# Performance work log

Hardware: AMD Instinct MI355X
Metric: run time of the kernel (lower is better)

## Reference

```python
import jax, jax.numpy as jnp
import numpy as np

E = 500_000
NODE_DIM = 128
EDGE_DIM = 128
GLOB_DIM = 64
NUM_GRAPHS = 64
HIDDEN = 4 * EDGE_DIM  # 512
IN_DIM = 2 * NODE_DIM + EDGE_DIM + GLOB_DIM  # 448
EPS = 1e-5


def setup_inputs() -> dict:
    key = jax.random.key(0)
    ks = jax.random.split(key, 12)
    src = jax.random.normal(ks[0], (E, NODE_DIM), dtype=jnp.float32)
    dest = jax.random.normal(ks[1], (E, NODE_DIM), dtype=jnp.float32)
    edge_attr = jax.random.normal(ks[2], (E, EDGE_DIM), dtype=jnp.float32)
    u = jax.random.normal(ks[3], (NUM_GRAPHS, GLOB_DIM), dtype=jnp.float32)
    batch = jnp.sort(jax.random.randint(ks[4], (E,), 0, NUM_GRAPHS, dtype=jnp.int32))
    # MLP params (kaiming-ish scale)
    W1 = jax.random.normal(ks[5], (IN_DIM, HIDDEN), dtype=jnp.float32) / np.sqrt(IN_DIM)
    b1 = jnp.zeros((HIDDEN,), dtype=jnp.float32)
    W2 = jax.random.normal(ks[6], (HIDDEN, EDGE_DIM), dtype=jnp.float32) / np.sqrt(HIDDEN)
    b2 = jnp.zeros((EDGE_DIM,), dtype=jnp.float32)
    # GraphNorm params
    gn_weight = jnp.ones((EDGE_DIM,), dtype=jnp.float32)
    gn_bias = jnp.zeros((EDGE_DIM,), dtype=jnp.float32)
    mean_scale = jnp.ones((EDGE_DIM,), dtype=jnp.float32)
    return {"src": src, "dest": dest, "edge_attr": edge_attr, "u": u, "batch": batch,
            "W1": W1, "b1": b1, "W2": W2, "b2": b2,
            "gn_weight": gn_weight, "gn_bias": gn_bias, "mean_scale": mean_scale}


def _graph_norm(x, batch, weight, bias, mean_scale):
    # per-graph mean
    cnt = jax.ops.segment_sum(jnp.ones((x.shape[0],), x.dtype), batch, num_segments=NUM_GRAPHS)
    cnt = jnp.maximum(cnt, 1.0)[:, None]  # [G,1]
    mean = jax.ops.segment_sum(x, batch, num_segments=NUM_GRAPHS) / cnt  # [G,D]
    out = x - mean[batch] * mean_scale
    var = jax.ops.segment_sum(out * out, batch, num_segments=NUM_GRAPHS) / cnt  # [G,D]
    std = jnp.sqrt(var + EPS)
    return out / std[batch] * weight + bias


def reference(src, dest, edge_attr, u, batch, W1, b1, W2, b2, gn_weight, gn_bias, mean_scale):
    # gather per-graph globals + concat: [E, 2*node+edge+glob]
    h = jnp.concatenate([src, dest, edge_attr, u[batch]], axis=1)
    h = jax.nn.relu(h @ W1 + b1) @ W2 + b2  # [E, edge_dim]
    out = _graph_norm(h + edge_attr, batch, gn_weight, gn_bias, mean_scale)
    return out  # dropout is identity in eval / p=0.0
```

## Files before the change

kernel.cpp:

```cpp
#include <hip/hip_runtime.h>
#include <hip/hip_bf16.h>
#include <stdint.h>

#define E_EDGES   500000
#define MBLK      32
#define NBLK      15625
#define EPSV      1e-5f

typedef unsigned short u16;
typedef __attribute__((ext_vector_type(8))) short short8;
typedef __attribute__((ext_vector_type(4))) float f32x4;
typedef __attribute__((ext_vector_type(2))) uint32_t u32x2;

__device__ __forceinline__ u16 f2bf(float f) {
  __hip_bfloat16 h = __float2bfloat16(f);
  return *(u16*)&h;
}
__device__ __forceinline__ uint32_t pk2bf(float lo, float hi) {
  return (uint32_t)f2bf(lo) | ((uint32_t)f2bf(hi) << 16);
}

__global__ void prep_weights(const float* __restrict__ W1, const float* __restrict__ W2,
                             u16* __restrict__ w1f, u16* __restrict__ w2f) {
  int idx = blockIdx.x * blockDim.x + threadIdx.x;
  if (idx < 32*14*64) {
    int lane = idx & 63; int t = idx >> 6; int k32 = t % 14; int n16 = t / 14;
    int n = n16*16 + (lane & 15); int k0 = k32*32 + (lane >> 4)*8;
    short8 pk;
#pragma unroll
    for (int j = 0; j < 8; ++j) pk[j] = (short)f2bf(W1[(size_t)(k0 + j)*512 + n]);
    *(short8*)&w1f[(size_t)idx * 8] = pk;
  } else if (idx < 32*14*64 + 8*16*64) {
    int i2 = idx - 32*14*64;
    int lane = i2 & 63; int t = i2 >> 6; int k32 = t % 16; int n16 = t / 16;
    int n = n16*16 + (lane & 15); int k0 = k32*32 + (lane >> 4)*8;
    short8 pk;
#pragma unroll
    for (int j = 0; j < 8; ++j) pk[j] = (short)f2bf(W2[(size_t)(k0 + j)*128 + n]);
    *(short8*)&w2f[(size_t)i2 * 8] = pk;
  }
}

#define SWZ16(row, byte) ((byte) ^ (((row) & 7) << 4))

__global__ __launch_bounds__(256, 4)
void fused_kernel(const float* __restrict__ srcp, const float* __restrict__ destp,
                  const float* __restrict__ edgep, const float* __restrict__ up,
                  const int* __restrict__ batch, const float* __restrict__ b1,
                  const float* __restrict__ b2,
                  const u16* __restrict__ w1f, const u16* __restrict__ w2f,
                  float* __restrict__ outp,
                  float* __restrict__ sums0, float* __restrict__ sums2,
                  float* __restrict__ cntsh, int nshard) {
  const int tid  = threadIdx.x;
  const int lane = tid & 63;
  const int w    = tid >> 6;
  const int l15  = lane & 15, l4 = lane >> 4;

  __shared__ __align__(16) u16 lds[32*512];
  char* ldsb = (char*)lds;

  const long grow0 = (long)blockIdx.x * MBLK;

  {
    const int srow = tid >> 3;
    const int c8   = (tid & 7) * 8;
    const long sgrow = grow0 + srow;
    const int  bat = batch[sgrow];
#pragma unroll
    for (int j = 0; j < 7; ++j) {
      const float* sp;
      if (j == 0)      sp = srcp  + sgrow*128 + c8;
      else if (j == 1) sp = srcp  + sgrow*128 + 64 + c8;
      else if (j == 2) sp = destp + sgrow*128 + c8;
      else if (j == 3) sp = destp + sgrow*128 + 64 + c8;
      else if (j == 4) sp = edgep + sgrow*128 + c8;
      else if (j == 5) sp = edgep + sgrow*128 + 64 + c8;
      else             sp = up + (size_t)bat*64 + c8;
      f32x4 t0 = *(const f32x4*)(sp);
      f32x4 t1 = *(const f32x4*)(sp + 4);
      u32x2 lohi0 = (u32x2){pk2bf(t0[0], t0[1]), pk2bf(t0[2], t0[3])};
      u32x2 lohi1 = (u32x2){pk2bf(t1[0], t1[1]), pk2bf(t1[2], t1[3])};
      char* dst = ldsb + srow*896 + SWZ16(srow, (j*64 + c8)*2);
      *(u32x2*)(dst)     = lohi0;
      *(u32x2*)(dst + 8) = lohi1;
    }
  }
  __syncthreads();

  f32x4 acc1[2][8];
#pragma unroll
  for (int nj = 0; nj < 8; ++nj) {
    float bv = b1[(w*8 + nj)*16 + l15];
    acc1[0][nj] = (f32x4){bv, bv, bv, bv};
    acc1[1][nj] = (f32x4){bv, bv, bv, bv};
  }

#pragma unroll
  for (int k32 = 0; k32 < 14; ++k32) {
    short8 a[2], b[8];
#pragma unroll
    for (int mi = 0; mi < 2; ++mi) {
      int row = mi*16 + l15;
      a[mi] = *(const short8*)(ldsb + row*896 + SWZ16(row, k32*64 + l4*16));
    }
#pragma unroll
    for (int nj = 0; nj < 8; ++nj)
      b[nj] = *(const short8*)&w1f[((size_t)((w*8 + nj)*14 + k32)*64 + lane)*8];
    __builtin_amdgcn_s_setprio(1);
#pragma unroll
    for (int mi = 0; mi < 2; ++mi)
#pragma unroll
      for (int nj = 0; nj < 8; ++nj)
        acc1[mi][nj] = __builtin_amdgcn_mfma_f32_16x16x32_bf16(a[mi], b[nj], acc1[mi][nj], 0, 0, 0);
    __builtin_amdgcn_s_setprio(0);
  }
  __syncthreads();

#pragma unroll
  for (int nj = 0; nj < 8; ++nj) {
    int n = (w*8 + nj)*16 + l15;
#pragma unroll
    for (int mi = 0; mi < 2; ++mi)
#pragma unroll
      for (int rr = 0; rr < 4; ++rr) {
        int row = mi*16 + l4*4 + rr;
        *(u16*)(ldsb + row*1024 + SWZ16(row, n*2)) = f2bf(fmaxf(acc1[mi][nj][rr], 0.f));
      }
  }
  __syncthreads();

  const int c4    = tid & 31;
  const int rbase = tid >> 5;
  f32x4 ebuf[4];
#pragma unroll
  for (int p = 0; p < 4; ++p)
    ebuf[p] = *(const f32x4*)(edgep + (grow0 + rbase + p*8)*128 + c4*4);

  f32x4 acc2[2][2];
#pragma unroll
  for (int nj = 0; nj < 2; ++nj) {
    float bv = b2[(w*2 + nj)*16 + l15];
    acc2[0][nj] = (f32x4){bv, bv, bv, bv};
    acc2[1][nj] = (f32x4){bv, bv, bv, bv};
  }

#pragma unroll
  for (int kb = 0; kb < 16; ++kb) {
    short8 hb[2], wfr[2];
#pragma unroll
    for (int mi = 0; mi < 2; ++mi) {
      int row = mi*16 + l15;
      hb[mi] = *(const short8*)(ldsb + row*1024 + SWZ16(row, kb*64 + l4*16));
    }
#pragma unroll
    for (int nj = 0; nj < 2; ++nj)
      wfr[nj] = *(const short8*)&w2f[(((size_t)((w*2 + nj)*16 + kb))*64 + lane)*8];
    __builtin_amdgcn_s_setprio(1);
#pragma unroll
    for (int mi = 0; mi < 2; ++mi)
#pragma unroll
      for (int nj = 0; nj < 2; ++nj)
        acc2[mi][nj] = __builtin_amdgcn_mfma_f32_16x16x32_bf16(hb[mi], wfr[nj], acc2[mi][nj], 0, 0, 0);
    __builtin_amdgcn_s_setprio(0);
  }
  __syncthreads();

#pragma unroll
  for (int mi = 0; mi < 2; ++mi)
#pragma unroll
    for (int nj = 0; nj < 2; ++nj) {
      int col = (w*2 + nj)*16 + l15;
#pragma unroll
      for (int rr = 0; rr < 4; ++rr) {
        int row = mi*16 + l4*4 + rr;
        *(float*)(ldsb + row*512 + SWZ16(row, col*4)) = acc2[mi][nj][rr];
      }
    }
  __syncthreads();

  const int g0 = batch[grow0];
  const int g1 = batch[grow0 + MBLK - 1];
  const int sh = blockIdx.x & (nshard - 1);

  if (g0 == g1) {
    f32x4 s = (f32x4){0,0,0,0}, s2 = (f32x4){0,0,0,0};
#pragma unroll
    for (int p = 0; p < 4; ++p) {
      int row = rbase + p*8;
      f32x4 y = *(const f32x4*)(ldsb + row*512 + SWZ16(row, c4*16));
      y = y + ebuf[p];
      *(f32x4*)(outp + (grow0 + row)*128 + c4*4) = y;
      s = s + y; s2 = s2 + y*y;
    }
    int slot = 16384 + (rbase*32 + c4)*32;
    *(f32x4*)(ldsb + slot)      = s;
    *(f32x4*)(ldsb + slot + 16) = s2;
    __syncthreads();
    int c4r = tid >> 3, stat = (tid >> 2) & 1, cq = tid & 3;
    float v = 0.f;
#pragma unroll
    for (int r = 0; r < 8; ++r)
      v += *(const float*)(ldsb + 16384 + (r*32 + c4r)*32 + stat*16 + cq*4);
    float* dst = stat ? sums2 : sums0;
    atomicAdd(&dst[(size_t)sh*8192 + g0*128 + c4r*4 + cq], v);
    if (tid == 0) atomicAdd(&cntsh[sh*64 + g0], (float)MBLK);
  } else {
    f32x4 s = (f32x4){0,0,0,0}, s2 = (f32x4){0,0,0,0};
    float rc = 0.f; int gcur = -1;
#pragma unroll
    for (int p = 0; p < 4; ++p) {
      int row = rbase + p*8;
      int g = batch[grow0 + row];
      if (g != gcur) {
        if (gcur >= 0) {
#pragma unroll
          for (int c = 0; c < 4; ++c) {
            atomicAdd(&sums0[(size_t)sh*8192 + gcur*128 + c4*4 + c], s[c]);
            atomicAdd(&sums2[(size_t)sh*8192 + gcur*128 + c4*4 + c], s2[c]);
          }
          if (c4 == 0) atomicAdd(&cntsh[sh*64 + gcur], rc);
        }
        gcur = g; s = (f32x4){0,0,0,0}; s2 = (f32x4){0,0,0,0}; rc = 0.f;
      }
      f32x4 y = *(const f32x4*)(ldsb + row*512 + SWZ16(row, c4*16));
      y = y + ebuf[p];
      *(f32x4*)(outp + (grow0 + row)*128 + c4*4) = y;
      s = s + y; s2 = s2 + y*y; rc += 1.f;
    }
#pragma unroll
    for (int c = 0; c < 4; ++c) {
      atomicAdd(&sums0[(size_t)sh*8192 + gcur*128 + c4*4 + c], s[c]);
      atomicAdd(&sums2[(size_t)sh*8192 + gcur*128 + c4*4 + c], s2[c]);
    }
    if (c4 == 0) atomicAdd(&cntsh[sh*64 + gcur], rc);
  }
}

__global__ void finalize_kernel(const float* __restrict__ sums0, const float* __restrict__ sums2,
                                const float* __restrict__ cntsh, int nshard,
                                const float* __restrict__ gnw, const float* __restrict__ gnb,
                                const float* __restrict__ ms,
                                float* __restrict__ scale, float* __restrict__ shift) {
  int idx = blockIdx.x*blockDim.x + threadIdx.x;
  if (idx >= 64*128) return;
  int g = idx >> 7, d = idx & 127;
  float s = 0.f, s2 = 0.f, c = 0.f;
  for (int sh = 0; sh < nshard; ++sh) {
    s  += sums0[(size_t)sh*8192 + idx];
    s2 += sums2[(size_t)sh*8192 + idx];
    c  += cntsh[sh*64 + g];
  }
  c = fmaxf(c, 1.0f);
  float mean = s / c;
  float mm = mean * ms[d];
  float var = fmaxf(s2 / c - 2.f*mm*mean + mm*mm, 0.f);
  float sc = gnw[d] / sqrtf(var + EPSV);
  scale[idx] = sc;
  shift[idx] = gnb[d] - mm*sc;
}

__global__ void norm_kernel(float* __restrict__ y, const int* __restrict__ batch,
                            const float* __restrict__ scale, const float* __restrict__ shift) {
  long i = (long)blockIdx.x*blockDim.x + threadIdx.x;
  const long n4 = (long)E_EDGES * 32;
  long stride = (long)gridDim.x*blockDim.x;
  for (; i < n4; i += stride) {
    long row = i >> 5;
    int dq = (int)(i & 31) << 2;
    int g = batch[row];
    f32x4 v = *(f32x4*)(y + i*4);
    f32x4 sc = *(const f32x4*)(scale + g*128 + dq);
    f32x4 sh = *(const f32x4*)(shift + g*128 + dq);
    v = v*sc + sh;
    *(f32x4*)(y + i*4) = v;
  }
}

extern "C" void kernel_launch(void* const* d_in, const int* in_sizes, int n_in,
                              void* d_out, int out_size, void* d_ws, size_t ws_size,
                              hipStream_t stream) {
  const float* srcp  = (const float*)d_in[0];
  const float* destp = (const float*)d_in[1];
  const float* edgep = (const float*)d_in[2];
  const float* up    = (const float*)d_in[3];
  const int*   batch = (const int*)d_in[4];
  const float* W1    = (const float*)d_in[5];
  const float* b1    = (const float*)d_in[6];
  const float* W2    = (const float*)d_in[7];
  const float* b2    = (const float*)d_in[8];
  const float* gnw   = (const float*)d_in[9];
  const float* gnb   = (const float*)d_in[10];
  const float* ms    = (const float*)d_in[11];
  float* outp = (float*)d_out;

  char* ws = (char*)d_ws;
  u16*   w1f   = (u16*)(ws + 0);
  u16*   w2f   = (u16*)(ws + 458752);
  float* scale = (float*)(ws + 589824);
  float* shift = (float*)(ws + 622592);
  float* cntsh = (float*)(ws + 655360);
  int nshard = 32;
  while (nshard > 1 && 663552 + (size_t)nshard*65536 > ws_size) nshard >>= 1;
  float* sums0 = (float*)(ws + 663552);
  float* sums2 = (float*)(ws + 663552 + (size_t)nshard*32768);

  hipMemsetAsync(ws + 655360, 0, 8192 + (size_t)nshard*65536, stream);
  prep_weights<<<dim3(144), dim3(256), 0, stream>>>(W1, W2, w1f, w2f);

  fused_kernel<<<dim3(NBLK), dim3(256), 0, stream>>>(srcp, destp, edgep, up, batch,
                                                     b1, b2, w1f, w2f, outp,
                                                     sums0, sums2, cntsh, nshard);

  finalize_kernel<<<dim3(32), dim3(256), 0, stream>>>(sums0, sums2, cntsh, nshard,
                                                      gnw, gnb, ms, scale, shift);
  norm_kernel<<<dim3(2048), dim3(256), 0, stream>>>(outp, batch, scale, shift);
}
```

Measured before the change: 580.7 us.

## Halve row tile and stream fp32 inputs into LDS via global_load_lds

Cuts the rows per block from 32 to 16, doubling the grid, and loads the concatenated fp32 input rows straight into LDS with the async global-to-LDS builtin instead of converting to bf16 through registers. The bf16 conversion now happens when A-fragments are read from LDS inside the first GEMM loop. Loops are partially unrolled and the setprio hints are dropped. Each block now reuses every weight-fragment load across half as many rows, so global and L2 weight traffic doubles. Boundary blocks also issue atomics per row rather than per graph run.

```diff
diff --git a/kernel.cpp b/kernel.cpp
--- a/kernel.cpp
+++ b/kernel.cpp
@@ -3,14 +3,17 @@
 #include <stdint.h>
 
 #define E_EDGES   500000
-#define MBLK      32
-#define NBLK      15625
+#define MBLK      16
+#define NBLK      31250
 #define EPSV      1e-5f
+#define HOFF      0
+#define YOFF2     16384
+#define STOFF2    24576
 
 typedef unsigned short u16;
 typedef __attribute__((ext_vector_type(8))) short short8;
 typedef __attribute__((ext_vector_type(4))) float f32x4;
-typedef __attribute__((ext_vector_type(2))) uint32_t u32x2;
+typedef __attribute__((ext_vector_type(4))) uint32_t u32x4;
 
 __device__ __forceinline__ u16 f2bf(float f) {
   __hip_bfloat16 h = __float2bfloat16(f);
@@ -18,6 +21,10 @@
 }
 __device__ __forceinline__ uint32_t pk2bf(float lo, float hi) {
   return (uint32_t)f2bf(lo) | ((uint32_t)f2bf(hi) << 16);
+}
+__device__ __forceinline__ void gload_lds16(const void* g, void* l) {
+  __builtin_amdgcn_global_load_lds((const __attribute__((address_space(1))) uint32_t*)g,
+                                   (__attribute__((address_space(3))) uint32_t*)l, 16, 0, 0);
 }
 
 __global__ void prep_weights(const float* __restrict__ W1, const float* __restrict__ W2,
@@ -57,63 +64,48 @@
   const int w    = tid >> 6;
   const int l15  = lane & 15, l4 = lane >> 4;
 
-  __shared__ __align__(16) u16 lds[32*512];
-  char* ldsb = (char*)lds;
+  __shared__ __align__(16) char ldsb[32768];
 
   const long grow0 = (long)blockIdx.x * MBLK;
 
-  {
-    const int srow = tid >> 3;
-    const int c8   = (tid & 7) * 8;
-    const long sgrow = grow0 + srow;
-    const int  bat = batch[sgrow];
-#pragma unroll
-    for (int j = 0; j < 7; ++j) {
-      const float* sp;
-      if (j == 0)      sp = srcp  + sgrow*128 + c8;
-      else if (j == 1) sp = srcp  + sgrow*128 + 64 + c8;
-      else if (j == 2) sp = destp + sgrow*128 + c8;
-      else if (j == 3) sp = destp + sgrow*128 + 64 + c8;
-      else if (j == 4) sp = edgep + sgrow*128 + c8;
-      else if (j == 5) sp = edgep + sgrow*128 + 64 + c8;
-      else             sp = up + (size_t)bat*64 + c8;
-      f32x4 t0 = *(const f32x4*)(sp);
-      f32x4 t1 = *(const f32x4*)(sp + 4);
-      u32x2 lohi0 = (u32x2){pk2bf(t0[0], t0[1]), pk2bf(t0[2], t0[3])};
-      u32x2 lohi1 = (u32x2){pk2bf(t1[0], t1[1]), pk2bf(t1[2], t1[3])};
-      char* dst = ldsb + srow*896 + SWZ16(srow, (j*64 + c8)*2);
-      *(u32x2*)(dst)     = lohi0;
-      *(u32x2*)(dst + 8) = lohi1;
-    }
-  }
-  __syncthreads();
-
-  f32x4 acc1[2][8];
+#pragma unroll
+  for (int i = 0; i < 7; ++i) {
+    int s   = i*4096 + tid*16;
+    int row = s / 1792;
+    int off = s - row*1792;
+    int soff = SWZ16(row, off);
+    int fo = soff >> 2;
+    const float* gp;
+    if (fo < 128)      gp = srcp  + (grow0 + row)*128 + fo;
+    else if (fo < 256) gp = destp + (grow0 + row)*128 + (fo - 128);
+    else if (fo < 384) gp = edgep + (grow0 + row)*128 + (fo - 256);
+    else               gp = up + (size_t)batch[grow0 + row]*64 + (fo - 384);
+    gload_lds16(gp, ldsb + s);
+  }
+  __syncthreads();
+
+  f32x4 acc1[8];
 #pragma unroll
   for (int nj = 0; nj < 8; ++nj) {
     float bv = b1[(w*8 + nj)*16 + l15];
-    acc1[0][nj] = (f32x4){bv, bv, bv, bv};
-    acc1[1][nj] = (f32x4){bv, bv, bv, bv};
-  }
-
-#pragma unroll
+    acc1[nj] = (f32x4){bv, bv, bv, bv};
+  }
+
+#pragma unroll 2
   for (int k32 = 0; k32 < 14; ++k32) {
-    short8 a[2], b[8];
-#pragma unroll
-    for (int mi = 0; mi < 2; ++mi) {
-      int row = mi*16 + l15;
-      a[mi] = *(const short8*)(ldsb + row*896 + SWZ16(row, k32*64 + l4*16));
-    }
+    int cb = k32*128 + l4*32;
+    f32x4 x0 = *(const f32x4*)(ldsb + l15*1792 + SWZ16(l15, cb));
+    f32x4 x1 = *(const f32x4*)(ldsb + l15*1792 + SWZ16(l15, cb + 16));
+    u32x4 ap = (u32x4){pk2bf(x0[0], x0[1]), pk2bf(x0[2], x0[3]),
+                       pk2bf(x1[0], x1[1]), pk2bf(x1[2], x1[3])};
+    short8 a = *(short8*)&ap;
+    short8 b[8];
 #pragma unroll
     for (int nj = 0; nj < 8; ++nj)
       b[nj] = *(const short8*)&w1f[((size_t)((w*8 + nj)*14 + k32)*64 + lane)*8];
-    __builtin_amdgcn_s_setprio(1);
-#pragma unroll
-    for (int mi = 0; mi < 2; ++mi)
-#pragma unroll
-      for (int nj = 0; nj < 8; ++nj)
-        acc1[mi][nj] = __builtin_amdgcn_mfma_f32_16x16x32_bf16(a[mi], b[nj], acc1[mi][nj], 0, 0, 0);
-    __builtin_amdgcn_s_setprio(0);
+#pragma unroll
+    for (int nj = 0; nj < 8; ++nj)
+      acc1[nj] = __builtin_amdgcn_mfma_f32_16x16x32_bf16(a, b[nj], acc1[nj], 0, 0, 0);
   }
   __syncthreads();
 
@@ -121,62 +113,48 @@
   for (int nj = 0; nj < 8; ++nj) {
     int n = (w*8 + nj)*16 + l15;
 #pragma unroll
-    for (int mi = 0; mi < 2; ++mi)
-#pragma unroll
-      for (int rr = 0; rr < 4; ++rr) {
-        int row = mi*16 + l4*4 + rr;
-        *(u16*)(ldsb + row*1024 + SWZ16(row, n*2)) = f2bf(fmaxf(acc1[mi][nj][rr], 0.f));
-      }
+    for (int rr = 0; rr < 4; ++rr) {
+      int row = l4*4 + rr;
+      *(u16*)(ldsb + HOFF + row*1024 + SWZ16(row, n*2)) = f2bf(fmaxf(acc1[nj][rr], 0.f));
+    }
   }
   __syncthreads();
 
   const int c4    = tid & 31;
   const int rbase = tid >> 5;
-  f32x4 ebuf[4];
-#pragma unroll
-  for (int p = 0; p < 4; ++p)
+  f32x4 ebuf[2];
+#pragma unroll
+  for (int p = 0; p < 2; ++p)
     ebuf[p] = *(const f32x4*)(edgep + (grow0 + rbase + p*8)*128 + c4*4);
 
-  f32x4 acc2[2][2];
+  f32x4 acc2[2];
 #pragma unroll
   for (int nj = 0; nj < 2; ++nj) {
     float bv = b2[(w*2 + nj)*16 + l15];
-    acc2[0][nj] = (f32x4){bv, bv, bv, bv};
-    acc2[1][nj] = (f32x4){bv, bv, bv, bv};
-  }
-
-#pragma unroll
+    acc2[nj] = (f32x4){bv, bv, bv, bv};
+  }
+
+#pragma unroll 4
   for (int kb = 0; kb < 16; ++kb) {
-    short8 hb[2], wfr[2];
-#pragma unroll
-    for (int mi = 0; mi < 2; ++mi) {
-      int row = mi*16 + l15;
-      hb[mi] = *(const short8*)(ldsb + row*1024 + SWZ16(row, kb*64 + l4*16));
-    }
+    short8 hb = *(const short8*)(ldsb + HOFF + l15*1024 + SWZ16(l15, kb*64 + l4*16));
+    short8 wfr[2];
 #pragma unroll
     for (int nj = 0; nj < 2; ++nj)
       wfr[nj] = *(const short8*)&w2f[(((size_t)((w*2 + nj)*16 + kb))*64 + lane)*8];
-    __builtin_amdgcn_s_setprio(1);
-#pragma unroll
-    for (int mi = 0; mi < 2; ++mi)
-#pragma unroll
-      for (int nj = 0; nj < 2; ++nj)
-        acc2[mi][nj] = __builtin_amdgcn_mfma_f32_16x16x32_bf16(hb[mi], wfr[nj], acc2[mi][nj], 0, 0, 0);
-    __builtin_amdgcn_s_setprio(0);
-  }
-  __syncthreads();
-
-#pragma unroll
-  for (int mi = 0; mi < 2; ++mi)
-#pragma unroll
-    for (int nj = 0; nj < 2; ++nj) {
-      int col = (w*2 + nj)*16 + l15;
-#pragma unroll
-      for (int rr = 0; rr < 4; ++rr) {
-        int row = mi*16 + l4*4 + rr;
-        *(float*)(ldsb + row*512 + SWZ16(row, col*4)) = acc2[mi][nj][rr];
-      }
-    }
+#pragma unroll
+    for (int nj = 0; nj < 2; ++nj)
+      acc2[nj] = __builtin_amdgcn_mfma_f32_16x16x32_bf16(hb, wfr[nj], acc2[nj], 0, 0, 0);
+  }
+
+#pragma unroll
+  for (int nj = 0; nj < 2; ++nj) {
+    int col = (w*2 + nj)*16 + l15;
+#pragma unroll
+    for (int rr = 0; rr < 4; ++rr) {
+      int row = l4*4 + rr;
+      *(float*)(ldsb + YOFF2 + row*512 + SWZ16(row, col*4)) = acc2[nj][rr];
+    }
+  }
   __syncthreads();
 
   const int g0 = batch[grow0];
@@ -186,14 +164,14 @@
   if (g0 == g1) {
     f32x4 s = (f32x4){0,0,0,0}, s2 = (f32x4){0,0,0,0};
 #pragma unroll
-    for (int p = 0; p < 4; ++p) {
+    for (int p = 0; p < 2; ++p) {
       int row = rbase + p*8;
-      f32x4 y = *(const f32x4*)(ldsb + row*512 + SWZ16(row, c4*16));
+      f32x4 y = *(const f32x4*)(ldsb + YOFF2 + row*512 + SWZ16(row, c4*16));
       y = y + ebuf[p];
       *(f32x4*)(outp + (grow0 + row)*128 + c4*4) = y;
       s = s + y; s2 = s2 + y*y;
     }
-    int slot = 16384 + (rbase*32 + c4)*32;
+    int slot = STOFF2 + (rbase*32 + c4)*32;
     *(f32x4*)(ldsb + slot)      = s;
     *(f32x4*)(ldsb + slot + 16) = s2;
     __syncthreads();
@@ -201,39 +179,25 @@
     float v = 0.f;
 #pragma unroll
     for (int r = 0; r < 8; ++r)
-      v += *(const float*)(ldsb + 16384 + (r*32 + c4r)*32 + stat*16 + cq*4);
+      v += *(const float*)(ldsb + STOFF2 + (r*32 + c4r)*32 + stat*16 + cq*4);
     float* dst = stat ? sums2 : sums0;
     atomicAdd(&dst[(size_t)sh*8192 + g0*128 + c4r*4 + cq], v);
     if (tid == 0) atomicAdd(&cntsh[sh*64 + g0], (float)MBLK);
   } else {
-    f32x4 s = (f32x4){0,0,0,0}, s2 = (f32x4){0,0,0,0};
-    float rc = 0.f; int gcur = -1;
-#pragma unroll
-    for (int p = 0; p < 4; ++p) {
+#pragma unroll
+    for (int p = 0; p < 2; ++p) {
       int row = rbase + p*8;
       int g = batch[grow0 + row];
-      if (g != gcur) {
-        if (gcur >= 0) {
-#pragma unroll
-          for (int c = 0; c < 4; ++c) {
-            atomicAdd(&sums0[(size_t)sh*8192 + gcur*128 + c4*4 + c], s[c]);
-            atomicAdd(&sums2[(size_t)sh*8192 + gcur*128 + c4*4 + c], s2[c]);
-          }
-          if (c4 == 0) atomicAdd(&cntsh[sh*64 + gcur], rc);
-        }
-        gcur = g; s = (f32x4){0,0,0,0}; s2 = (f32x4){0,0,0,0}; rc = 0.f;
-      }
-      f32x4 y = *(const f32x4*)(ldsb + row*512 + SWZ16(row, c4*16));
+      f32x4 y = *(const f32x4*)(ldsb + YOFF2 + row*512 + SWZ16(row, c4*16));
       y = y + ebuf[p];
       *(f32x4*)(outp + (grow0 + row)*128 + c4*4) = y;
-      s = s + y; s2 = s2 + y*y; rc += 1.f;
-    }
-#pragma unroll
-    for (int c = 0; c < 4; ++c) {
-      atomicAdd(&sums0[(size_t)sh*8192 + gcur*128 + c4*4 + c], s[c]);
-      atomicAdd(&sums2[(size_t)sh*8192 + gcur*128 + c4*4 + c], s2[c]);
-    }
-    if (c4 == 0) atomicAdd(&cntsh[sh*64 + gcur], rc);
+#pragma unroll
+      for (int c = 0; c < 4; ++c) {
+        atomicAdd(&sums0[(size_t)sh*8192 + g*128 + c4*4 + c], y[c]);
+        atomicAdd(&sums2[(size_t)sh*8192 + g*128 + c4*4 + c], y[c]*y[c]);
+      }
+      if (c4 == 0) atomicAdd(&cntsh[sh*64 + g], 1.0f);
+    }
   }
 }
 
```

Result: slower. 1.013 ms (+74.5%).
